# Optimization experiments

Measured on AMD Instinct MI355X. Metric: run time of the kernel, lower is better.

## Reference

```python
import jax, jax.numpy as jnp
import numpy as np

B, S, D_MODEL, D_MEM, N_HEADS, NU = 8, 2048, 1024, 1024, 16, 3
D_HEAD = D_MODEL // N_HEADS            # 64
D_KEY = 2 * NU * (D_MEM // N_HEADS)    # 384


def _to_heads(x, n_heads):
    b, s, d = x.shape
    return x.reshape(b, s, n_heads, d // n_heads).transpose(0, 2, 1, 3)


def _dpfp(x, nu):
    # Deterministic Positive Feature Projection: (..., d) -> (..., 2*nu*d)
    x = jnp.concatenate([jax.nn.relu(x), jax.nn.relu(-x)], axis=-1)
    rolled = jnp.concatenate([jnp.roll(x, j, axis=-1) for j in range(1, nu + 1)], axis=-1)
    rep = jnp.concatenate([x] * nu, axis=-1)
    return rep * rolled


def setup_inputs() -> dict:
    key = jax.random.key(0)
    k0, k1, k2, k3, k4 = jax.random.split(key, 5)
    mem_tokens = jax.random.normal(k0, (B, S, D_MODEL), dtype=jnp.float32)
    # nn.Linear(in, out) weight shape is [out, in]
    W_mk = jax.random.normal(k1, (D_MEM, D_MODEL), dtype=jnp.float32) * 0.02
    W_mv = jax.random.normal(k2, (D_MODEL, D_MODEL), dtype=jnp.float32) * 0.02
    W_mb = jax.random.normal(k3, (D_MODEL, D_MODEL), dtype=jnp.float32) * 0.02
    W_mem = jax.random.normal(k4, (B, N_HEADS, D_KEY, D_HEAD), dtype=jnp.float32) * 0.01
    z = jnp.ones((B, N_HEADS, D_KEY), dtype=jnp.float32)
    return {"mem_tokens": mem_tokens, "W_mk": W_mk, "W_mv": W_mv, "W_mb": W_mb,
            "W_mem": W_mem, "z": z}


def reference(mem_tokens, W_mk, W_mv, W_mb, W_mem, z):
    # key projection + DPFP feature map
    k = _to_heads(mem_tokens @ W_mk.T, N_HEADS)          # [b,h,s,d_mem/h]
    mk = _dpfp(k, NU)                                     # [b,h,s,d_key]
    norm = jnp.linalg.norm(mk, axis=-1, keepdims=True)
    mk = mk / jnp.maximum(norm, 1e-12)                    # F.normalize(p=2)

    new_mv = _to_heads(mem_tokens @ W_mv.T, N_HEADS)      # [b,h,s,d_head]

    # retrieve previous values (first_seg=False, use_denom=True path)
    num = jnp.einsum('bhsk,bhkd->bhsd', mk, W_mem)
    denom = jnp.einsum('bhk,bhsk->bhs', z, mk)[..., None] + 1e-5
    prev_mv = num / denom

    mv = new_mv - prev_mv
    mb = _to_heads(jax.nn.sigmoid(mem_tokens @ W_mb.T), N_HEADS)

    # gating=True einsum: 'ihjk,ihjt,ihjt->ihkt'
    associations = jnp.einsum('bhsk,bhsd,bhsd->bhkd', mk, mv, mb)
    return W_mem + associations
```

## Files before the change

### kernel.cpp

```cpp
#include <hip/hip_runtime.h>
#include <hip/hip_bf16.h>

#define B_ 8
#define S_ 2048
#define DM 1024
#define H_ 16
#define DH 64
#define DK 384

#define AS3 __attribute__((address_space(3)))
#define AS1 __attribute__((address_space(1)))
typedef unsigned int u32;

typedef __attribute__((ext_vector_type(8))) short bf16x8;
typedef __attribute__((ext_vector_type(4))) short bf16x4;
typedef __attribute__((ext_vector_type(4))) float f32x4;

static __device__ __forceinline__ ushort f2b(float f) {
  __hip_bfloat16 h = __float2bfloat16(f);
  return *reinterpret_cast<ushort*>(&h);
}
static __device__ __forceinline__ float b2f(ushort u) {
  __hip_bfloat16 h;
  *reinterpret_cast<ushort*>(&h) = u;
  return __bfloat162float(h);
}

__global__ __launch_bounds__(256) void k_cvt(
    const float* __restrict__ X, const float* __restrict__ Wk,
    const float* __restrict__ Wv, const float* __restrict__ Wb,
    ushort* __restrict__ Xb, ushort* __restrict__ Wball) {
  const int total = 2097152 + 3 * 131072;
  int c = blockIdx.x * 256 + threadIdx.x;
  const int stride = gridDim.x * 256;
  for (; c < total; c += stride) {
    const float* s;
    ushort* d;
    size_t off;
    if (c < 2097152) { s = X; d = Xb; off = (size_t)c; }
    else {
      int cc = c - 2097152;
      int wsel = cc >> 17;
      off = (size_t)(cc & 131071);
      s = wsel == 0 ? Wk : (wsel == 1 ? Wv : Wb);
      d = Wball + (size_t)wsel * (DM * DM);
    }
    float4 a = *(const float4*)(s + off * 8);
    float4 b = *(const float4*)(s + off * 8 + 4);
    ushort u[8] = { f2b(a.x), f2b(a.y), f2b(a.z), f2b(a.w),
                    f2b(b.x), f2b(b.y), f2b(b.z), f2b(b.w) };
    *(uint4*)(d + off * 8) = *(uint4*)u;
  }
}

__global__ __launch_bounds__(256) void k_proj(
    const ushort* __restrict__ Xb, const ushort* __restrict__ Wball,
    ushort* __restrict__ kvb) {
  __shared__ ushort SH[4 * 8192];
  ushort* As = SH;
  ushort* Bs = SH + 2 * 8192;
  const int t = threadIdx.x, lane = t & 63, w = t >> 6;
  const int wm = w >> 1, wn = w & 1;
  const int bid = blockIdx.x + (blockIdx.y << 7) + (blockIdx.z << 10);
  const int c = bid & 7, r = bid >> 3;
  const int xb = c * 16 + (r & 15);
  const int rest = r >> 4;
  const int yb = rest & 7, zb = rest >> 3;
  const int m0 = xb * 128;
  const int n0 = yb * 128;
  const int wsel = zb;
  const ushort* Wmat = Wball + (size_t)wsel * (DM * DM);
  ushort* out = kvb + (size_t)wsel * ((size_t)B_ * H_ * S_ * DH);

  const int rowst = (lane >> 3);
  const int colsw = ((lane & 7) ^ rowst) << 3;

  auto STAGE = [&](int buf, int k0) {
    #pragma unroll
    for (int j = 0; j < 4; j++) {
      int row = (w * 4 + j) * 8 + rowst;
      __builtin_amdgcn_global_load_lds(
          (const AS1 u32*)(Xb + (size_t)(m0 + row) * DM + k0 + colsw),
          (AS3 u32*)(As + buf * 8192 + (w * 4 + j) * 512), 16, 0, 0);
      __builtin_amdgcn_global_load_lds(
          (const AS1 u32*)(Wmat + (size_t)(n0 + row) * DM + k0 + colsw),
          (AS3 u32*)(Bs + buf * 8192 + (w * 4 + j) * 512), 16, 0, 0);
    }
  };

  f32x4 acc[4][4] = {};
  STAGE(0, 0);
  __syncthreads();
  int cur = 0;
  for (int kt = 0; kt < 16; kt++) {
    if (kt < 15) STAGE(cur ^ 1, (kt + 1) * 64);
    const ushort* Ab = As + cur * 8192;
    const ushort* Bb = Bs + cur * 8192;
    #pragma unroll
    for (int kk2 = 0; kk2 < 2; kk2++) {
      const int csw = (((lane >> 4) + 4 * kk2) ^ (lane & 7)) << 3;
      bf16x8 af[4], bfr[4];
      #pragma unroll
      for (int mi = 0; mi < 4; mi++)
        af[mi] = *(const bf16x8*)&Ab[(wm * 64 + mi * 16 + (lane & 15)) * 64 + csw];
      #pragma unroll
      for (int ni = 0; ni < 4; ni++)
        bfr[ni] = *(const bf16x8*)&Bb[(wn * 64 + ni * 16 + (lane & 15)) * 64 + csw];
      #pragma unroll
      for (int mi = 0; mi < 4; mi++)
        #pragma unroll
        for (int ni = 0; ni < 4; ni++)
          acc[mi][ni] = __builtin_amdgcn_mfma_f32_16x16x32_bf16(af[mi], bfr[ni], acc[mi][ni], 0, 0, 0);
    }
    __syncthreads();
    cur ^= 1;
  }

  ushort (*Cb)[136] = (ushort (*)[136])SH;
  #pragma unroll
  for (int mi = 0; mi < 4; mi++)
    #pragma unroll
    for (int ni = 0; ni < 4; ni++)
      #pragma unroll
      for (int rr = 0; rr < 4; rr++) {
        float val = acc[mi][ni][rr];
        if (wsel == 2) val = 1.0f / (1.0f + __expf(-val));
        Cb[wm * 64 + mi * 16 + (lane >> 4) * 4 + rr]
          [wn * 64 + ni * 16 + (lane & 15)] = f2b(val);
      }
  __syncthreads();
  #pragma unroll
  for (int q = 0; q < 8; q++) {
    int idx = q * 256 + t;
    int lm = idx >> 4;
    int c16 = idx & 15;
    int m = m0 + lm;
    int b = m >> 11, s = m & 2047;
    int o0 = n0 + c16 * 8;
    int h = o0 >> 6, d = o0 & 63;
    *(uint4*)(out + (((size_t)(b * H_ + h)) * S_ + s) * DH + d) =
        *(uint4*)&Cb[lm][c16 * 8];
  }
}

__global__ __launch_bounds__(512) void k_fused6(
    const ushort* __restrict__ Kb, const ushort* __restrict__ Vb,
    const ushort* __restrict__ Bgb, const float* __restrict__ Wmem,
    const float* __restrict__ z, ushort* __restrict__ part) {
  __shared__ u32 mkLd[32][192];
  __shared__ ushort mkT[384][36];
  __shared__ ushort gLT[64][36];
  __shared__ ushort zL[384];
  const int t = threadIdx.x, l = t & 63, w = t >> 6;
  const int l15 = l & 15, lq = l >> 4;
  const int bh = blockIdx.y, seg = blockIdx.x;
  const size_t rowbase = (size_t)bh * S_;
  const int mi = w >> 2, ni = w & 3;
  const int dcol = ni * 16 + l15;

  for (int cc = t; cc < DK; cc += 512) {
    int u = cc >> 7, p = (cc & 127) >> 1, par = cc & 1;
    zL[cc] = f2b(z[(size_t)bh * DK + u * 128 + par * 64 + p]);
  }

  const float* Wm = Wmem + (size_t)bh * (DK * DH);
  bf16x8 bw[12];
  #pragma unroll
  for (int k0i = 0; k0i < 12; k0i++) {
    bf16x8 tmp;
    #pragma unroll
    for (int j = 0; j < 8; j++) {
      int cc = k0i * 32 + lq * 8 + j;
      int u = cc >> 7, p = (cc & 127) >> 1, par = cc & 1;
      tmp[j] = (short)f2b(Wm[(size_t)(u * 128 + par * 64 + p) * DH + dcol]);
    }
    bw[k0i] = tmp;
  }

  f32x4 acc[3][4] = {};
  ushort kreg[4], vreg[4], breg[4];

  auto LOADCH = [&](int ch) {
    const int s0 = seg * 512 + ch * 32;
    #pragma unroll
    for (int r = 0; r < 4; r++)
      kreg[r] = Kb[(rowbase + s0 + w * 4 + r) * DH + l];
    #pragma unroll
    for (int rr = 0; rr < 4; rr++) {
      size_t ga = (rowbase + s0 + mi * 16 + lq * 4 + rr) * DH + dcol;
      vreg[rr] = Vb[ga];
      breg[rr] = Bgb[ga];
    }
  };

  LOADCH(0);
  __syncthreads();

  for (int ch = 0; ch < 16; ch++) {
    float xpv[4], xnv[4];
    u32 pks[4];
    #pragma unroll
    for (int r = 0; r < 4; r++) {
      float kv = b2f(kreg[r]);
      xpv[r] = fmaxf(kv, 0.f);
      xnv[r] = fmaxf(-kv, 0.f);
      pks[r] = (u32)f2b(xpv[r]) | ((u32)f2b(xnv[r]) << 16);
    }
    ushort4 mp[6];
    #pragma unroll
    for (int u = 0; u < 3; u++) {
      int ie = (l - u - 1) & 127;
      int sl = ie & 63;
      bool sw = ie >= 64;
      #pragma unroll
      for (int r = 0; r < 4; r++) {
        u32 pp = (u32)__shfl((int)pks[r], sl);
        float ps = b2f((ushort)(pp & 0xffff));
        float ns = b2f((ushort)(pp >> 16));
        float xbe = sw ? ns : ps;
        float xbo = sw ? ps : ns;
        ushort bve = f2b(xpv[r] * xbe);
        ushort bvo = f2b(xnv[r] * xbo);
        int row = w * 4 + r;
        mkLd[row][(u * 64 + l) ^ ((row & 7) << 2)] = (u32)bve | ((u32)bvo << 16);
        ((ushort*)&mp[2 * u])[r] = bve;
        ((ushort*)&mp[2 * u + 1])[r] = bvo;
      }
    }
    #pragma unroll
    for (int tt = 0; tt < 6; tt++)
      *(ushort4*)&mkT[l + 64 * tt][w * 4] = mp[tt];
    __syncthreads();

    const u32* mkrow = &mkLd[mi * 16 + l15][0];
    const int xr = (l15 & 7) << 2;
    f32x4 an0 = {}, an1 = {}, gacc = {}, zacc = {};
    #pragma unroll
    for (int k0i = 0; k0i < 12; k0i += 2) {
      bf16x8 afA = *(const bf16x8*)(mkrow + ((k0i * 16 + lq * 4) ^ xr));
      bf16x8 afB = *(const bf16x8*)(mkrow + (((k0i + 1) * 16 + lq * 4) ^ xr));
      bf16x8 zfA = *(const bf16x8*)&zL[k0i * 32 + lq * 8];
      bf16x8 zfB = *(const bf16x8*)&zL[(k0i + 1) * 32 + lq * 8];
      an0 = __builtin_amdgcn_mfma_f32_16x16x32_bf16(afA, bw[k0i], an0, 0, 0, 0);
      an1 = __builtin_amdgcn_mfma_f32_16x16x32_bf16(afB, bw[k0i + 1], an1, 0, 0, 0);
      gacc = __builtin_amdgcn_mfma_f32_16x16x32_bf16(afA, afA, gacc, 0, 0, 0);
      gacc = __builtin_amdgcn_mfma_f32_16x16x32_bf16(afB, afB, gacc, 0, 0, 0);
      zacc = __builtin_amdgcn_mfma_f32_16x16x32_bf16(afA, zfA, zacc, 0, 0, 0);
      zacc = __builtin_amdgcn_mfma_f32_16x16x32_bf16(afB, zfB, zacc, 0, 0, 0);
    }
    f32x4 an = an0 + an1;
    float ssqv[4];
    #pragma unroll
    for (int rr = 0; rr < 4; rr++)
      ssqv[rr] = __shfl(gacc[rr], (lq << 4) + lq * 4 + rr);
    {
      ushort4 gp;
      #pragma unroll
      for (int rr = 0; rr < 4; rr++) {
        float inv = 1.0f / fmaxf(sqrtf(ssqv[rr]), 1e-12f);
        float rden = 1.0f / (inv * zacc[rr] + 1e-5f);
        float prev = an[rr] * inv * rden;
        float g = (b2f(vreg[rr]) - prev) * b2f(breg[rr]);
        ((ushort*)&gp)[rr] = f2b(g * inv);
      }
      *(ushort4*)&gLT[dcol][mi * 16 + lq * 4] = gp;
    }
    __syncthreads();

    if (ch < 15) LOADCH(ch + 1);

    {
      bf16x8 bfr[4];
      #pragma unroll
      for (int n2 = 0; n2 < 4; n2++) {
        bf16x4 blo = *(const bf16x4*)&gLT[n2 * 16 + l15][lq * 8];
        bf16x4 bhi = *(const bf16x4*)&gLT[n2 * 16 + l15][lq * 8 + 4];
        bfr[n2] = __builtin_shufflevector(blo, bhi, 0, 1, 2, 3, 4, 5, 6, 7);
      }
      #pragma unroll
      for (int m2 = 0; m2 < 3; m2++) {
        bf16x4 alo = *(const bf16x4*)&mkT[w * 48 + m2 * 16 + l15][lq * 8];
        bf16x4 ahi = *(const bf16x4*)&mkT[w * 48 + m2 * 16 + l15][lq * 8 + 4];
        bf16x8 af = __builtin_shufflevector(alo, ahi, 0, 1, 2, 3, 4, 5, 6, 7);
        #pragma unroll
        for (int n2 = 0; n2 < 4; n2++)
          acc[m2][n2] = __builtin_amdgcn_mfma_f32_16x16x32_bf16(af, bfr[n2], acc[m2][n2], 0, 0, 0);
      }
    }
    __syncthreads();
  }

  ushort* pb = part + ((size_t)bh * 4 + seg) * (DK * DH);
  #pragma unroll
  for (int m2 = 0; m2 < 3; m2++)
    #pragma unroll
    for (int n2 = 0; n2 < 4; n2++)
      #pragma unroll
      for (int rc = 0; rc < 4; rc++)
        pb[(size_t)(w * 48 + m2 * 16 + lq * 4 + rc) * DH + n2 * 16 + l15] =
            f2b(acc[m2][n2][rc]);
}

__global__ __launch_bounds__(256) void k_reduce(
    const float* __restrict__ Wmem, const ushort* __restrict__ part,
    float* __restrict__ out) {
  size_t i4 = (size_t)blockIdx.x * 256 + threadIdx.x;
  int bh = (int)(i4 / 6144);
  size_t r4 = i4 - (size_t)bh * 6144;
  float4 acc = *(const float4*)(Wmem + i4 * 4);
  #pragma unroll
  for (int k = 0; k < 4; k++) {
    const ushort* pp = part + ((size_t)bh * 4 + k) * (DK * DH) + r4 * 4;
    ushort4 pv = *(const ushort4*)pp;
    acc.x += b2f(pv.x);
    acc.y += b2f(pv.y);
    acc.z += b2f(pv.z);
    acc.w += b2f(pv.w);
  }
  *(float4*)(out + i4 * 4) = acc;
}

extern "C" void kernel_launch(void* const* d_in, const int* in_sizes, int n_in,
                              void* d_out, int out_size, void* d_ws, size_t ws_size,
                              hipStream_t stream) {
  const float* X  = (const float*)d_in[0];
  const float* Wk = (const float*)d_in[1];
  const float* Wv = (const float*)d_in[2];
  const float* Wb = (const float*)d_in[3];
  const float* Wm = (const float*)d_in[4];
  const float* z  = (const float*)d_in[5];
  float* out = (float*)d_out;
  char* ws = (char*)d_ws;

  ushort* Xb    = (ushort*)(ws);
  ushort* Wball = (ushort*)(ws + 33554432ull);
  ushort* kvb   = (ushort*)(ws + 39845888ull);
  ushort* part  = (ushort*)(ws);
  ushort* Kb  = kvb;
  ushort* Vb  = kvb + (size_t)B_ * H_ * S_ * DH;
  ushort* Bgb = kvb + 2ull * (size_t)B_ * H_ * S_ * DH;

  k_cvt   <<<dim3(2048), 256, 0, stream>>>(X, Wk, Wv, Wb, Xb, Wball);
  k_proj  <<<dim3(128, 8, 3), 256, 0, stream>>>(Xb, Wball, kvb);
  k_fused6<<<dim3(4, B_ * H_), 512, 0, stream>>>(Kb, Vb, Bgb, Wm, z, part);
  k_reduce<<<dim3(3072), 256, 0, stream>>>(Wm, part, out);
}
```

Before: 257.0 us.

## Halve projection GEMM K-tile, drop LDS swizzle, reorder block-to-tile mapping

The projection GEMM now stages 32-wide K slices instead of 64, which halves LDS usage per block (about 34 KB instead of 64 KB) and may let more blocks share a CU. The XOR swizzle on LDS columns is removed in favour of a plain row-major layout with 4 lanes per row. Block indices are remapped so consecutive blocks walk the N tiles of one M row-block, which is meant to improve L2 reuse of the activation rows. The trade-off is twice as many barriers per K loop and possible LDS bank conflicts on fragment reads now that the swizzle is gone.

```diff
diff --git a/kernel.cpp b/kernel.cpp
--- a/kernel.cpp
+++ b/kernel.cpp
@@ -56,35 +56,35 @@
 __global__ __launch_bounds__(256) void k_proj(
     const ushort* __restrict__ Xb, const ushort* __restrict__ Wball,
     ushort* __restrict__ kvb) {
-  __shared__ ushort SH[4 * 8192];
+  __shared__ ushort SH[17408];
   ushort* As = SH;
-  ushort* Bs = SH + 2 * 8192;
+  ushort* Bs = SH + 8192;
   const int t = threadIdx.x, lane = t & 63, w = t >> 6;
   const int wm = w >> 1, wn = w & 1;
+  const int l15 = lane & 15, lq = lane >> 4;
   const int bid = blockIdx.x + (blockIdx.y << 7) + (blockIdx.z << 10);
   const int c = bid & 7, r = bid >> 3;
-  const int xb = c * 16 + (r & 15);
-  const int rest = r >> 4;
-  const int yb = rest & 7, zb = rest >> 3;
-  const int m0 = xb * 128;
-  const int n0 = yb * 128;
+  const int zb = r >> 7;
+  const int rem = r & 127;
+  const int mgrp = rem >> 3;
+  const int nb = rem & 7;
+  const int m0 = (c * 16 + mgrp) * 128;
+  const int n0 = nb * 128;
   const int wsel = zb;
   const ushort* Wmat = Wball + (size_t)wsel * (DM * DM);
   ushort* out = kvb + (size_t)wsel * ((size_t)B_ * H_ * S_ * DH);
 
-  const int rowst = (lane >> 3);
-  const int colsw = ((lane & 7) ^ rowst) << 3;
-
   auto STAGE = [&](int buf, int k0) {
     #pragma unroll
-    for (int j = 0; j < 4; j++) {
-      int row = (w * 4 + j) * 8 + rowst;
+    for (int j = 0; j < 2; j++) {
+      int row = (t >> 2) + j * 64;
+      int col8 = (t & 3) * 8;
       __builtin_amdgcn_global_load_lds(
-          (const AS1 u32*)(Xb + (size_t)(m0 + row) * DM + k0 + colsw),
-          (AS3 u32*)(As + buf * 8192 + (w * 4 + j) * 512), 16, 0, 0);
+          (const AS1 u32*)(Xb + (size_t)(m0 + row) * DM + k0 + col8),
+          (AS3 u32*)(As + buf * 4096 + j * 2048 + t * 8), 16, 0, 0);
       __builtin_amdgcn_global_load_lds(
-          (const AS1 u32*)(Wmat + (size_t)(n0 + row) * DM + k0 + colsw),
-          (AS3 u32*)(Bs + buf * 8192 + (w * 4 + j) * 512), 16, 0, 0);
+          (const AS1 u32*)(Wmat + (size_t)(n0 + row) * DM + k0 + col8),
+          (AS3 u32*)(Bs + buf * 4096 + j * 2048 + t * 8), 16, 0, 0);
     }
   };
 
@@ -92,26 +92,22 @@
   STAGE(0, 0);
   __syncthreads();
   int cur = 0;
-  for (int kt = 0; kt < 16; kt++) {
-    if (kt < 15) STAGE(cur ^ 1, (kt + 1) * 64);
-    const ushort* Ab = As + cur * 8192;
-    const ushort* Bb = Bs + cur * 8192;
-    #pragma unroll
-    for (int kk2 = 0; kk2 < 2; kk2++) {
-      const int csw = (((lane >> 4) + 4 * kk2) ^ (lane & 7)) << 3;
-      bf16x8 af[4], bfr[4];
-      #pragma unroll
-      for (int mi = 0; mi < 4; mi++)
-        af[mi] = *(const bf16x8*)&Ab[(wm * 64 + mi * 16 + (lane & 15)) * 64 + csw];
+  for (int kt = 0; kt < 32; kt++) {
+    if (kt < 31) STAGE(cur ^ 1, (kt + 1) * 32);
+    const ushort* Ab = As + cur * 4096;
+    const ushort* Bb = Bs + cur * 4096;
+    bf16x8 af[4], bfr[4];
+    #pragma unroll
+    for (int mi = 0; mi < 4; mi++)
+      af[mi] = *(const bf16x8*)&Ab[(wm * 64 + mi * 16 + l15) * 32 + lq * 8];
+    #pragma unroll
+    for (int ni = 0; ni < 4; ni++)
+      bfr[ni] = *(const bf16x8*)&Bb[(wn * 64 + ni * 16 + l15) * 32 + lq * 8];
+    #pragma unroll
+    for (int mi = 0; mi < 4; mi++)
       #pragma unroll
       for (int ni = 0; ni < 4; ni++)
-        bfr[ni] = *(const bf16x8*)&Bb[(wn * 64 + ni * 16 + (lane & 15)) * 64 + csw];
-      #pragma unroll
-      for (int mi = 0; mi < 4; mi++)
-        #pragma unroll
-        for (int ni = 0; ni < 4; ni++)
-          acc[mi][ni] = __builtin_amdgcn_mfma_f32_16x16x32_bf16(af[mi], bfr[ni], acc[mi][ni], 0, 0, 0);
-    }
+        acc[mi][ni] = __builtin_amdgcn_mfma_f32_16x16x32_bf16(af[mi], bfr[ni], acc[mi][ni], 0, 0, 0);
     __syncthreads();
     cur ^= 1;
   }
@@ -125,8 +121,7 @@
       for (int rr = 0; rr < 4; rr++) {
         float val = acc[mi][ni][rr];
         if (wsel == 2) val = 1.0f / (1.0f + __expf(-val));
-        Cb[wm * 64 + mi * 16 + (lane >> 4) * 4 + rr]
-          [wn * 64 + ni * 16 + (lane & 15)] = f2b(val);
+        Cb[wm * 64 + mi * 16 + lq * 4 + rr][wn * 64 + ni * 16 + l15] = f2b(val);
       }
   __syncthreads();
   #pragma unroll
```

New measurement: 274.4 us. 1.07x slower.
